# Kernel optimization log

Measured on AMD Instinct MI355X. Metric: run time of the kernel, lower is better.

## Reference

```python
import jax, jax.numpy as jnp
import numpy as np

B, C, F_IN, F_OUT = 4096, 63, 250, 250
NEG_SLOPE = 0.2  # GATConv default negative_slope


def setup_inputs() -> dict:
    key = jax.random.key(0)
    ks = jax.random.split(key, 5)
    return {
        "x": jax.random.normal(ks[0], (B, 1, C, F_IN), dtype=jnp.float32),
        "W": jax.random.normal(ks[1], (F_IN, F_OUT), dtype=jnp.float32) / np.sqrt(F_IN),
        "att_src": jax.random.normal(ks[2], (F_OUT,), dtype=jnp.float32) / np.sqrt(F_OUT),
        "att_dst": jax.random.normal(ks[3], (F_OUT,), dtype=jnp.float32) / np.sqrt(F_OUT),
        "bias": jax.random.normal(ks[4], (F_OUT,), dtype=jnp.float32) * 0.01,
    }


def reference(x, W, att_src, att_dst, bias):
    # x: [B, 1, C, F_in] -> per-batch graph of C=63 nodes, fully connected
    # (all i!=j edges plus GATConv's default self-loops => dense C x C attention).
    h = jnp.einsum("bcf,fo->bco", x[:, 0], W)          # [B, C, F_out] node embeddings
    a_s = jnp.einsum("bco,o->bc", h, att_src)           # per-source score
    a_d = jnp.einsum("bco,o->bc", h, att_dst)           # per-destination score
    # e[b, dst, src] = leakyrelu(a_s[src] + a_d[dst]); softmax over sources per dst
    e = jax.nn.leaky_relu(a_s[:, None, :] + a_d[:, :, None], NEG_SLOPE)  # [B, C, C]
    alpha = jax.nn.softmax(e, axis=-1)
    out = jnp.einsum("bds,bso->bdo", alpha, h) + bias   # [B, C, F_out]
    return out[:, None]                                  # [B, 1, C, F_out]
```

## Files before the change

kernel.cpp:

```cpp
#include <hip/hip_runtime.h>
#include <hip/hip_bf16.h>

typedef __bf16 bf16;
typedef __attribute__((ext_vector_type(8))) __bf16 bf16x8;
typedef __attribute__((ext_vector_type(2))) __bf16 bf16x2;
typedef __attribute__((ext_vector_type(4))) float f32x4;
typedef __attribute__((ext_vector_type(4))) unsigned int uint4v;

#define C_NODES 63
#define F_DIM   250
#define NEG_SLOPE 0.2f
#define BS 8

#define ROWB      1040
#define SLAB      0
#define OFF_AS    65536
#define OFF_AD    65792
#define ALPHA_B   66048
#define LDS_BYTES 74240

__device__ __forceinline__ int swz(int a) { return a ^ ((a >> 3) & 0x70); }

typedef const __attribute__((address_space(1))) void* gas_t;
typedef __attribute__((address_space(3))) void* las_t;
__device__ __forceinline__ void dma16(const void* g, void* l) {
    __builtin_amdgcn_global_load_lds((gas_t)g, (las_t)l, 16, 0, 0);
}

__device__ __forceinline__ void bar_lgkm() {
    asm volatile("s_waitcnt lgkmcnt(0)" ::: "memory");
    __builtin_amdgcn_s_barrier();
    __builtin_amdgcn_sched_barrier(0);
}

extern "C" __global__ __launch_bounds__(256)
void gat_prep(const float* __restrict__ W, const float* __restrict__ att_src,
              const float* __restrict__ att_dst, bf16* __restrict__ Wp) {
    int i = blockIdx.x * 256 + threadIdx.x;
    int tile = i >> 9;
    int ln   = (i >> 3) & 63;
    int j    = i & 7;
    int kt = tile >> 4, nt = tile & 15;
    int k = kt * 32 + (ln >> 4) * 8 + j;
    int n = nt * 16 + (ln & 15);
    float v = 0.f;
    if (k < F_DIM) {
        if (n < F_DIM) {
            v = W[k * F_DIM + n];
        } else if (n == F_DIM || n == F_DIM + 1) {
            const float* att = (n == F_DIM) ? att_src : att_dst;
            float s = 0.f;
            for (int o = 0; o < F_DIM; ++o) s = fmaf(W[k * F_DIM + o], att[o], s);
            v = s;
        }
    }
    Wp[i] = (bf16)v;
}

extern "C" __global__ __launch_bounds__(512, 4)
void gat_main(const float* __restrict__ x, const bf16* __restrict__ Wp,
              const float* __restrict__ bias, float* __restrict__ out)
{
    __shared__ __align__(16) unsigned char smem[LDS_BYTES];
    const int tid  = threadIdx.x;
    const int lane = tid & 63;
    const int w    = tid >> 6;
    const int fl   = lane & 15;
    const int fh   = lane >> 4;
    const int b0   = blockIdx.x * BS;

    const bf16x8* wpv = (const bf16x8*)Wp;

    float bv0, bv1;
    { int f = w * 32 + fl;      bv0 = (f < F_DIM) ? bias[f] : 0.f;
      f += 16;                  bv1 = (f < F_DIM) ? bias[f] : 0.f; }

    if (tid < 63) {
        *(unsigned long long*)(smem + SLAB + tid * ROWB + 1000) = 0ull;
        *(f32x4*)(smem + SLAB + tid * ROWB + 1008) = (f32x4){0.f, 0.f, 0.f, 0.f};
    }

    {
        const float* xb = x + (size_t)b0 * (C_NODES * F_DIM);
        float2 tl0 = {0.f, 0.f};
        if (tid < 63) tl0 = *(const float2*)(xb + tid * F_DIM + 248);
#pragma unroll
        for (int rr = 0; rr < 8; ++rr) {
            int r = w * 8 + rr;
            if (r < 63 && lane < 62)
                dma16(xb + r * F_DIM + lane * 4, smem + SLAB + r * ROWB);
        }
        if (tid < 63) *(float2*)(smem + SLAB + tid * ROWB + 992) = tl0;
    }
    asm volatile("s_waitcnt vmcnt(0)" ::: "memory");
    bar_lgkm();

#pragma unroll 1
    for (int i = 0; i < BS; ++i) {
        const int b = b0 + i;
        const float* xnext = x + (size_t)(b + 1) * (C_NODES * F_DIM);

        float2 tl = {0.f, 0.f};
        if (i + 1 < BS && tid < 63) tl = *(const float2*)(xnext + tid * F_DIM + 248);

        f32x4 gacc[4][2];
#pragma unroll
        for (int mt = 0; mt < 4; ++mt) {
            gacc[mt][0] = (f32x4){0.f, 0.f, 0.f, 0.f};
            gacc[mt][1] = (f32x4){0.f, 0.f, 0.f, 0.f};
        }
#pragma unroll 2
        for (int kt = 0; kt < 8; ++kt) {
            bf16x8 bw0 = wpv[(kt * 16 + w * 2)     * 64 + lane];
            bf16x8 bw1 = wpv[(kt * 16 + w * 2 + 1) * 64 + lane];
#pragma unroll
            for (int mt = 0; mt < 4; ++mt) {
                int row = mt * 16 + fl;
                bf16x8 af;
                if (row < C_NODES) {
                    const f32x4* p = (const f32x4*)(smem + SLAB + row * ROWB + kt * 128 + fh * 32);
                    f32x4 lo = p[0], hi = p[1];
                    af = (bf16x8){ (bf16)lo.x, (bf16)lo.y, (bf16)lo.z, (bf16)lo.w,
                                   (bf16)hi.x, (bf16)hi.y, (bf16)hi.z, (bf16)hi.w };
                } else {
                    af = (bf16x8){(bf16)0.f,(bf16)0.f,(bf16)0.f,(bf16)0.f,
                                  (bf16)0.f,(bf16)0.f,(bf16)0.f,(bf16)0.f};
                }
                gacc[mt][0] = __builtin_amdgcn_mfma_f32_16x16x32_bf16(af, bw0, gacc[mt][0], 0, 0, 0);
                gacc[mt][1] = __builtin_amdgcn_mfma_f32_16x16x32_bf16(af, bw1, gacc[mt][1], 0, 0, 0);
            }
        }
        if (w == 7 && (fl == 10 || fl == 11)) {
            float* dst = (float*)(smem + (fl == 10 ? OFF_AS : OFF_AD));
#pragma unroll
            for (int mt = 0; mt < 4; ++mt) {
                f32x4 v = gacc[mt][1];
#pragma unroll
                for (int q = 0; q < 4; ++q) dst[mt * 16 + fh * 4 + q] = v[q];
            }
        }
        bar_lgkm();

        if (i + 1 < BS) {
#pragma unroll
            for (int rr = 0; rr < 8; ++rr) {
                int r = w * 8 + rr;
                if (r < 63 && lane < 62)
                    dma16(xnext + r * F_DIM + lane * 4, smem + SLAB + r * ROWB);
            }
        }
        unsigned int pk[4][2][2];
#pragma unroll
        for (int mt = 0; mt < 4; ++mt)
#pragma unroll
            for (int nti = 0; nti < 2; ++nti) {
                f32x4 v = gacc[mt][nti];
                bf16x2 p0 = { (bf16)v.x, (bf16)v.y };
                bf16x2 p1 = { (bf16)v.z, (bf16)v.w };
                pk[mt][nti][0] = __builtin_bit_cast(unsigned int, p0);
                pk[mt][nti][1] = __builtin_bit_cast(unsigned int, p1);
            }
        const int LA = ((fh & 1) << 5) + fl;
        const int LB = LA + 16;
        const bool fhHi = (fh & 2) != 0;
        uint4v hb[2][2];
#pragma unroll
        for (int nti = 0; nti < 2; ++nti)
#pragma unroll
            for (int kt2 = 0; kt2 < 2; ++kt2) {
                unsigned int u[4];
#pragma unroll
                for (int h = 0; h < 2; ++h) {
                    unsigned int a0 = __shfl(pk[kt2 * 2][nti][h],     LA);
                    unsigned int a1 = __shfl(pk[kt2 * 2 + 1][nti][h], LA);
                    u[h] = fhHi ? a1 : a0;
                    unsigned int c0 = __shfl(pk[kt2 * 2][nti][h],     LB);
                    unsigned int c1 = __shfl(pk[kt2 * 2 + 1][nti][h], LB);
                    u[2 + h] = fhHi ? c1 : c0;
                }
                hb[nti][kt2] = (uint4v){u[0], u[1], u[2], u[3]};
            }
        {
            const float* AS  = (const float*)(smem + OFF_AS);
            const float* ADp = (const float*)(smem + OFF_AD);
            int d = tid >> 3;
            int c = tid & 7;
            float ad_v = ADp[d];
            f32x4 a0 = *(const f32x4*)(AS + c * 8);
            f32x4 a1 = *(const f32x4*)(AS + c * 8 + 4);
            float p[8];
#pragma unroll
            for (int k = 0; k < 4; ++k) {
                float e;
                e = a0[k] + ad_v; p[k]     = (e > 0.f) ? e : NEG_SLOPE * e;
                e = a1[k] + ad_v; p[4 + k] = (e > 0.f) ? e : NEG_SLOPE * e;
            }
            if (c == 7) p[7] = -3.0e38f;
            float md = p[0];
#pragma unroll
            for (int k = 1; k < 8; ++k) md = fmaxf(md, p[k]);
            md = fmaxf(md, __shfl_xor(md, 1));
            md = fmaxf(md, __shfl_xor(md, 2));
            md = fmaxf(md, __shfl_xor(md, 4));
            float sum = 0.f;
#pragma unroll
            for (int k = 0; k < 8; ++k) { p[k] = __expf(p[k] - md); sum += p[k]; }
            sum += __shfl_xor(sum, 1);
            sum += __shfl_xor(sum, 2);
            sum += __shfl_xor(sum, 4);
            float rz = 1.f / sum;
            bf16x8 pkv;
#pragma unroll
            for (int k = 0; k < 8; ++k) pkv[k] = (bf16)(p[k] * rz);
            *(bf16x8*)(smem + swz(ALPHA_B + d * 128 + c * 16)) = pkv;
        }
        if (i + 1 < BS && tid < 63)
            *(float2*)(smem + SLAB + tid * ROWB + 992) = tl;
        bar_lgkm();

#pragma unroll
        for (int mt = 0; mt < 4; ++mt) {
            gacc[mt][0] = (f32x4){0.f, 0.f, 0.f, 0.f};
            gacc[mt][1] = (f32x4){0.f, 0.f, 0.f, 0.f};
        }
#pragma unroll
        for (int ks = 0; ks < 2; ++ks) {
            int kk = ks * 32 + fh * 8;
            bf16x8 h0 = __builtin_bit_cast(bf16x8, hb[0][ks]);
            bf16x8 h1 = __builtin_bit_cast(bf16x8, hb[1][ks]);
#pragma unroll
            for (int mt = 0; mt < 4; ++mt) {
                bf16x8 aal = *(const bf16x8*)(smem + swz(ALPHA_B + (mt * 16 + fl) * 128 + kk * 2));
                gacc[mt][0] = __builtin_amdgcn_mfma_f32_16x16x32_bf16(aal, h0, gacc[mt][0], 0, 0, 0);
                gacc[mt][1] = __builtin_amdgcn_mfma_f32_16x16x32_bf16(aal, h1, gacc[mt][1], 0, 0, 0);
            }
        }
        float* ob = out + (size_t)b * (C_NODES * F_DIM);
#pragma unroll
        for (int mt = 0; mt < 4; ++mt) {
#pragma unroll
            for (int q = 0; q < 4; ++q) {
                int r = mt * 16 + fh * 4 + q;
                if (r < C_NODES) {
                    int f = w * 32 + fl;
                    ob[r * F_DIM + f] = gacc[mt][0][q] + bv0;
                    f += 16;
                    if (f < F_DIM) ob[r * F_DIM + f] = gacc[mt][1][q] + bv1;
                }
            }
        }
        if (i + 1 < BS) {
            asm volatile("s_waitcnt vmcnt(32)" ::: "memory");
            bar_lgkm();
        }
    }
}

extern "C" void kernel_launch(void* const* d_in, const int* in_sizes, int n_in,
                              void* d_out, int out_size, void* d_ws, size_t ws_size,
                              hipStream_t stream) {
    const float* x       = (const float*)d_in[0];
    const float* W       = (const float*)d_in[1];
    const float* att_src = (const float*)d_in[2];
    const float* att_dst = (const float*)d_in[3];
    const float* bias    = (const float*)d_in[4];
    float* out = (float*)d_out;
    bf16* Wp = (bf16*)d_ws;

    gat_prep<<<256, 256, 0, stream>>>(W, att_src, att_dst, Wp);
    gat_main<<<512, 512, 0, stream>>>(x, Wp, bias, out);
}
```

Baseline: 139.6 us.

## Double-buffer x slabs and software-pipeline the next graph's projection GEMM

Adds a second LDS slab so x for graph i+2 is DMA'd while graph i is processed. The projection GEMM for the next graph is moved to the end of the current iteration, after the attention GEMM. Graphs per block rise from 8 to 16 and the grid is halved, aiming to hide global-load latency behind compute. LDS per block roughly doubles and launch bounds drop to 2, so fewer blocks fit per CU. The explicit vmcnt waits before the slabs are read are removed, which risks reading LDS before the DMA has landed.

```diff
diff --git a/kernel.cpp b/kernel.cpp
--- a/kernel.cpp
+++ b/kernel.cpp
@@ -10,14 +10,15 @@
 #define C_NODES 63
 #define F_DIM   250
 #define NEG_SLOPE 0.2f
-#define BS 8
+#define BS 16
 
 #define ROWB      1040
-#define SLAB      0
-#define OFF_AS    65536
-#define OFF_AD    65792
-#define ALPHA_B   66048
-#define LDS_BYTES 74240
+#define SLAB0     0
+#define SLAB1     65536
+#define OFF_AS    131072
+#define OFF_AD    131328
+#define ALPHA_B   131584
+#define LDS_BYTES 139776
 
 __device__ __forceinline__ int swz(int a) { return a ^ ((a >> 3) & 0x70); }
 
@@ -57,7 +58,7 @@
     Wp[i] = (bf16)v;
 }
 
-extern "C" __global__ __launch_bounds__(512, 4)
+extern "C" __global__ __launch_bounds__(512, 2)
 void gat_main(const float* __restrict__ x, const bf16* __restrict__ Wp,
               const float* __restrict__ bias, float* __restrict__ out)
 {
@@ -76,8 +77,10 @@
       f += 16;                  bv1 = (f < F_DIM) ? bias[f] : 0.f; }
 
     if (tid < 63) {
-        *(unsigned long long*)(smem + SLAB + tid * ROWB + 1000) = 0ull;
-        *(f32x4*)(smem + SLAB + tid * ROWB + 1008) = (f32x4){0.f, 0.f, 0.f, 0.f};
+        *(unsigned long long*)(smem + SLAB0 + tid * ROWB + 1000) = 0ull;
+        *(f32x4*)(smem + SLAB0 + tid * ROWB + 1008) = (f32x4){0.f, 0.f, 0.f, 0.f};
+        *(unsigned long long*)(smem + SLAB1 + tid * ROWB + 1000) = 0ull;
+        *(f32x4*)(smem + SLAB1 + tid * ROWB + 1008) = (f32x4){0.f, 0.f, 0.f, 0.f};
     }
 
     {
@@ -88,65 +91,78 @@
         for (int rr = 0; rr < 8; ++rr) {
             int r = w * 8 + rr;
             if (r < 63 && lane < 62)
-                dma16(xb + r * F_DIM + lane * 4, smem + SLAB + r * ROWB);
-        }
-        if (tid < 63) *(float2*)(smem + SLAB + tid * ROWB + 992) = tl0;
-    }
-    asm volatile("s_waitcnt vmcnt(0)" ::: "memory");
+                dma16(xb + r * F_DIM + lane * 4, smem + SLAB0 + r * ROWB);
+        }
+        if (tid < 63) *(float2*)(smem + SLAB0 + tid * ROWB + 992) = tl0;
+    }
+    {
+        const float* xb = x + (size_t)(b0 + 1) * (C_NODES * F_DIM);
+        float2 tl1 = {0.f, 0.f};
+        if (tid < 63) tl1 = *(const float2*)(xb + tid * F_DIM + 248);
+#pragma unroll
+        for (int rr = 0; rr < 8; ++rr) {
+            int r = w * 8 + rr;
+            if (r < 63 && lane < 62)
+                dma16(xb + r * F_DIM + lane * 4, smem + SLAB1 + r * ROWB);
+        }
+        if (tid < 63) *(float2*)(smem + SLAB1 + tid * ROWB + 992) = tl1;
+    }
+    bar_lgkm();
+
+    f32x4 gacc[4][2];
+#pragma unroll
+    for (int mt = 0; mt < 4; ++mt) {
+        gacc[mt][0] = (f32x4){0.f, 0.f, 0.f, 0.f};
+        gacc[mt][1] = (f32x4){0.f, 0.f, 0.f, 0.f};
+    }
+#pragma unroll 2
+    for (int kt = 0; kt < 8; ++kt) {
+        bf16x8 bw0 = wpv[(kt * 16 + w * 2)     * 64 + lane];
+        bf16x8 bw1 = wpv[(kt * 16 + w * 2 + 1) * 64 + lane];
+#pragma unroll
+        for (int mt = 0; mt < 4; ++mt) {
+            int row = mt * 16 + fl;
+            bf16x8 af;
+            if (row < C_NODES) {
+                const f32x4* p = (const f32x4*)(smem + SLAB0 + row * ROWB + kt * 128 + fh * 32);
+                f32x4 lo = p[0], hi = p[1];
+                af = (bf16x8){ (bf16)lo.x, (bf16)lo.y, (bf16)lo.z, (bf16)lo.w,
+                               (bf16)hi.x, (bf16)hi.y, (bf16)hi.z, (bf16)hi.w };
+            } else {
+                af = (bf16x8){(bf16)0.f,(bf16)0.f,(bf16)0.f,(bf16)0.f,
+                              (bf16)0.f,(bf16)0.f,(bf16)0.f,(bf16)0.f};
+            }
+            gacc[mt][0] = __builtin_amdgcn_mfma_f32_16x16x32_bf16(af, bw0, gacc[mt][0], 0, 0, 0);
+            gacc[mt][1] = __builtin_amdgcn_mfma_f32_16x16x32_bf16(af, bw1, gacc[mt][1], 0, 0, 0);
+        }
+    }
+    if (w == 7 && (fl == 10 || fl == 11)) {
+        float* dst = (float*)(smem + (fl == 10 ? OFF_AS : OFF_AD));
+#pragma unroll
+        for (int mt = 0; mt < 4; ++mt) {
+            f32x4 v = gacc[mt][1];
+#pragma unroll
+            for (int q = 0; q < 4; ++q) dst[mt * 16 + fh * 4 + q] = v[q];
+        }
+    }
     bar_lgkm();
 
 #pragma unroll 1
     for (int i = 0; i < BS; ++i) {
         const int b = b0 + i;
-        const float* xnext = x + (size_t)(b + 1) * (C_NODES * F_DIM);
+        const int slabNext = ((i + 1) & 1) ? SLAB1 : SLAB0;
+        const int slabDma  = (i & 1) ? SLAB1 : SLAB0;
 
         float2 tl = {0.f, 0.f};
-        if (i + 1 < BS && tid < 63) tl = *(const float2*)(xnext + tid * F_DIM + 248);
-
-        f32x4 gacc[4][2];
-#pragma unroll
-        for (int mt = 0; mt < 4; ++mt) {
-            gacc[mt][0] = (f32x4){0.f, 0.f, 0.f, 0.f};
-            gacc[mt][1] = (f32x4){0.f, 0.f, 0.f, 0.f};
-        }
-#pragma unroll 2
-        for (int kt = 0; kt < 8; ++kt) {
-            bf16x8 bw0 = wpv[(kt * 16 + w * 2)     * 64 + lane];
-            bf16x8 bw1 = wpv[(kt * 16 + w * 2 + 1) * 64 + lane];
-#pragma unroll
-            for (int mt = 0; mt < 4; ++mt) {
-                int row = mt * 16 + fl;
-                bf16x8 af;
-                if (row < C_NODES) {
-                    const f32x4* p = (const f32x4*)(smem + SLAB + row * ROWB + kt * 128 + fh * 32);
-                    f32x4 lo = p[0], hi = p[1];
-                    af = (bf16x8){ (bf16)lo.x, (bf16)lo.y, (bf16)lo.z, (bf16)lo.w,
-                                   (bf16)hi.x, (bf16)hi.y, (bf16)hi.z, (bf16)hi.w };
-                } else {
-                    af = (bf16x8){(bf16)0.f,(bf16)0.f,(bf16)0.f,(bf16)0.f,
-                                  (bf16)0.f,(bf16)0.f,(bf16)0.f,(bf16)0.f};
-                }
-                gacc[mt][0] = __builtin_amdgcn_mfma_f32_16x16x32_bf16(af, bw0, gacc[mt][0], 0, 0, 0);
-                gacc[mt][1] = __builtin_amdgcn_mfma_f32_16x16x32_bf16(af, bw1, gacc[mt][1], 0, 0, 0);
-            }
-        }
-        if (w == 7 && (fl == 10 || fl == 11)) {
-            float* dst = (float*)(smem + (fl == 10 ? OFF_AS : OFF_AD));
-#pragma unroll
-            for (int mt = 0; mt < 4; ++mt) {
-                f32x4 v = gacc[mt][1];
-#pragma unroll
-                for (int q = 0; q < 4; ++q) dst[mt * 16 + fh * 4 + q] = v[q];
-            }
-        }
-        bar_lgkm();
-
-        if (i + 1 < BS) {
+        const bool dmaEn = (i + 2 < BS);
+        if (dmaEn) {
+            const float* xn = x + (size_t)(b + 2) * (C_NODES * F_DIM);
+            if (tid < 63) tl = *(const float2*)(xn + tid * F_DIM + 248);
 #pragma unroll
             for (int rr = 0; rr < 8; ++rr) {
                 int r = w * 8 + rr;
                 if (r < 63 && lane < 62)
-                    dma16(xnext + r * F_DIM + lane * 4, smem + SLAB + r * ROWB);
+                    dma16(xn + r * F_DIM + lane * 4, smem + slabDma + r * ROWB);
             }
         }
         unsigned int pk[4][2][2];
@@ -214,8 +230,11 @@
             for (int k = 0; k < 8; ++k) pkv[k] = (bf16)(p[k] * rz);
             *(bf16x8*)(smem + swz(ALPHA_B + d * 128 + c * 16)) = pkv;
         }
-        if (i + 1 < BS && tid < 63)
-            *(float2*)(smem + SLAB + tid * ROWB + 992) = tl;
+        if (dmaEn) {
+            if (tid < 63) *(float2*)(smem + slabDma + tid * ROWB + 992) = tl;
+        } else if (i + 1 < BS) {
+            asm volatile("s_waitcnt vmcnt(0)" ::: "memory");
+        }
         bar_lgkm();
 
 #pragma unroll
@@ -250,9 +269,43 @@
             }
         }
         if (i + 1 < BS) {
-            asm volatile("s_waitcnt vmcnt(32)" ::: "memory");
-            bar_lgkm();
-        }
+#pragma unroll
+            for (int mt = 0; mt < 4; ++mt) {
+                gacc[mt][0] = (f32x4){0.f, 0.f, 0.f, 0.f};
+                gacc[mt][1] = (f32x4){0.f, 0.f, 0.f, 0.f};
+            }
+#pragma unroll 2
+            for (int kt = 0; kt < 8; ++kt) {
+                bf16x8 bw0 = wpv[(kt * 16 + w * 2)     * 64 + lane];
+                bf16x8 bw1 = wpv[(kt * 16 + w * 2 + 1) * 64 + lane];
+#pragma unroll
+                for (int mt = 0; mt < 4; ++mt) {
+                    int row = mt * 16 + fl;
+                    bf16x8 af;
+                    if (row < C_NODES) {
+                        const f32x4* p = (const f32x4*)(smem + slabNext + row * ROWB + kt * 128 + fh * 32);
+                        f32x4 lo = p[0], hi = p[1];
+                        af = (bf16x8){ (bf16)lo.x, (bf16)lo.y, (bf16)lo.z, (bf16)lo.w,
+                                       (bf16)hi.x, (bf16)hi.y, (bf16)hi.z, (bf16)hi.w };
+                    } else {
+                        af = (bf16x8){(bf16)0.f,(bf16)0.f,(bf16)0.f,(bf16)0.f,
+                                      (bf16)0.f,(bf16)0.f,(bf16)0.f,(bf16)0.f};
+                    }
+                    gacc[mt][0] = __builtin_amdgcn_mfma_f32_16x16x32_bf16(af, bw0, gacc[mt][0], 0, 0, 0);
+                    gacc[mt][1] = __builtin_amdgcn_mfma_f32_16x16x32_bf16(af, bw1, gacc[mt][1], 0, 0, 0);
+                }
+            }
+            if (w == 7 && (fl == 10 || fl == 11)) {
+                float* dst = (float*)(smem + (fl == 10 ? OFF_AS : OFF_AD));
+#pragma unroll
+                for (int mt = 0; mt < 4; ++mt) {
+                    f32x4 v = gacc[mt][1];
+#pragma unroll
+                    for (int q = 0; q < 4; ++q) dst[mt * 16 + fh * 4 + q] = v[q];
+                }
+            }
+        }
+        bar_lgkm();
     }
 }
 
@@ -268,5 +321,5 @@
     bf16* Wp = (bf16*)d_ws;
 
     gat_prep<<<256, 256, 0, stream>>>(W, att_src, att_dst, Wp);
-    gat_main<<<512, 512, 0, stream>>>(x, Wp, bias, out);
-}
+    gat_main<<<256, 512, 0, stream>>>(x, Wp, bias, out);
+}
```

Result: slower. 144.4 us (+3.4%).

## Stage x as bf16 MFMA fragments in LDS and transpose h through LDS

Applied to the files above, without the earlier changes.

After each DMA of x, every wave converts its own fp32 rows once into a swizzled bf16 fragment layout in LDS, so the first GEMM loads A operands directly instead of converting fp32 on every k-step. The cross-lane shuffle transpose of h is replaced by a bf16 store to and reload from a swizzled LDS buffer. The batch count per block is doubled while the grid is halved. LDS use nearly doubles, which cuts resident blocks per CU and reduces latency hiding, and the per-row conversion adds an extra pass over LDS.

```diff
diff --git a/kernel.cpp b/kernel.cpp
--- a/kernel.cpp
+++ b/kernel.cpp
@@ -3,23 +3,28 @@
 
 typedef __bf16 bf16;
 typedef __attribute__((ext_vector_type(8))) __bf16 bf16x8;
+typedef __attribute__((ext_vector_type(4))) __bf16 bf16x4;
 typedef __attribute__((ext_vector_type(2))) __bf16 bf16x2;
 typedef __attribute__((ext_vector_type(4))) float f32x4;
-typedef __attribute__((ext_vector_type(4))) unsigned int uint4v;
 
 #define C_NODES 63
 #define F_DIM   250
 #define NEG_SLOPE 0.2f
-#define BS 8
+#define BS 16
 
 #define ROWB      1040
 #define SLAB      0
-#define OFF_AS    65536
-#define OFF_AD    65792
-#define ALPHA_B   66048
-#define LDS_BYTES 74240
+#define AFR_B     65536
+#define HSB       98304
+#define OFF_AS    130304
+#define OFF_AD    130560
+#define ALPHA_B   131072
+#define LDS_BYTES 139264
 
 __device__ __forceinline__ int swz(int a) { return a ^ ((a >> 3) & 0x70); }
+__device__ __forceinline__ int swzA(int a) {
+    return a ^ ((((a >> 8) & 3) ^ ((a >> 10) & 3)) << 4) ^ (((a >> 12) & 1) << 6);
+}
 
 typedef const __attribute__((address_space(1))) void* gas_t;
 typedef __attribute__((address_space(3))) void* las_t;
@@ -31,6 +36,22 @@
     asm volatile("s_waitcnt lgkmcnt(0)" ::: "memory");
     __builtin_amdgcn_s_barrier();
     __builtin_amdgcn_sched_barrier(0);
+}
+
+__device__ __forceinline__ void conv_rows(unsigned char* smem, int w, int lane) {
+#pragma unroll
+    for (int rr = 0; rr < 8; ++rr) {
+        int r = w * 8 + rr;
+        if (r < C_NODES) {
+            f32x4 v = *(const f32x4*)(smem + SLAB + r * ROWB + lane * 16);
+            int c = lane * 4;
+            int dl = (r & 15) | (((c >> 3) & 3) << 4);
+            int base = AFR_B + swzA((((r >> 4) * 8 + (c >> 5)) << 10)
+                                    + dl * 16 + (c & 4) * 2);
+            bf16x4 o = { (bf16)v.x, (bf16)v.y, (bf16)v.z, (bf16)v.w };
+            *(bf16x4*)(smem + base) = o;
+        }
+    }
 }
 
 extern "C" __global__ __launch_bounds__(256)
@@ -57,7 +78,7 @@
     Wp[i] = (bf16)v;
 }
 
-extern "C" __global__ __launch_bounds__(512, 4)
+extern "C" __global__ __launch_bounds__(512, 2)
 void gat_main(const float* __restrict__ x, const bf16* __restrict__ Wp,
               const float* __restrict__ bias, float* __restrict__ out)
 {
@@ -78,6 +99,10 @@
     if (tid < 63) {
         *(unsigned long long*)(smem + SLAB + tid * ROWB + 1000) = 0ull;
         *(f32x4*)(smem + SLAB + tid * ROWB + 1008) = (f32x4){0.f, 0.f, 0.f, 0.f};
+    } else if (tid < 96) {
+        int idx = tid - 64;
+        int base = AFR_B + swzA(((24 + (idx >> 2)) << 10) + ((((idx & 3) << 4) | 15) * 16));
+        *(f32x4*)(smem + base) = (f32x4){0.f, 0.f, 0.f, 0.f};
     }
 
     {
@@ -93,15 +118,15 @@
         if (tid < 63) *(float2*)(smem + SLAB + tid * ROWB + 992) = tl0;
     }
     asm volatile("s_waitcnt vmcnt(0)" ::: "memory");
+    __syncthreads();
+    conv_rows(smem, w, lane);
     bar_lgkm();
 
 #pragma unroll 1
     for (int i = 0; i < BS; ++i) {
         const int b = b0 + i;
+        const bool pfen = (i + 1 < BS);
         const float* xnext = x + (size_t)(b + 1) * (C_NODES * F_DIM);
-
-        float2 tl = {0.f, 0.f};
-        if (i + 1 < BS && tid < 63) tl = *(const float2*)(xnext + tid * F_DIM + 248);
 
         f32x4 gacc[4][2];
 #pragma unroll
@@ -115,17 +140,8 @@
             bf16x8 bw1 = wpv[(kt * 16 + w * 2 + 1) * 64 + lane];
 #pragma unroll
             for (int mt = 0; mt < 4; ++mt) {
-                int row = mt * 16 + fl;
-                bf16x8 af;
-                if (row < C_NODES) {
-                    const f32x4* p = (const f32x4*)(smem + SLAB + row * ROWB + kt * 128 + fh * 32);
-                    f32x4 lo = p[0], hi = p[1];
-                    af = (bf16x8){ (bf16)lo.x, (bf16)lo.y, (bf16)lo.z, (bf16)lo.w,
-                                   (bf16)hi.x, (bf16)hi.y, (bf16)hi.z, (bf16)hi.w };
-                } else {
-                    af = (bf16x8){(bf16)0.f,(bf16)0.f,(bf16)0.f,(bf16)0.f,
-                                  (bf16)0.f,(bf16)0.f,(bf16)0.f,(bf16)0.f};
-                }
+                bf16x8 af = *(const bf16x8*)(smem + AFR_B
+                                + swzA(((mt * 8 + kt) << 10) + lane * 16));
                 gacc[mt][0] = __builtin_amdgcn_mfma_f32_16x16x32_bf16(af, bw0, gacc[mt][0], 0, 0, 0);
                 gacc[mt][1] = __builtin_amdgcn_mfma_f32_16x16x32_bf16(af, bw1, gacc[mt][1], 0, 0, 0);
             }
@@ -141,7 +157,9 @@
         }
         bar_lgkm();
 
-        if (i + 1 < BS) {
+        float2 tl = {0.f, 0.f};
+        if (pfen) {
+            if (tid < 63) tl = *(const float2*)(xnext + tid * F_DIM + 248);
 #pragma unroll
             for (int rr = 0; rr < 8; ++rr) {
                 int r = w * 8 + rr;
@@ -149,37 +167,19 @@
                     dma16(xnext + r * F_DIM + lane * 4, smem + SLAB + r * ROWB);
             }
         }
-        unsigned int pk[4][2][2];
-#pragma unroll
-        for (int mt = 0; mt < 4; ++mt)
+#pragma unroll
+        for (int mt = 0; mt < 4; ++mt) {
+            int s0 = mt * 16 + fh * 4;
 #pragma unroll
             for (int nti = 0; nti < 2; ++nti) {
-                f32x4 v = gacc[mt][nti];
-                bf16x2 p0 = { (bf16)v.x, (bf16)v.y };
-                bf16x2 p1 = { (bf16)v.z, (bf16)v.w };
-                pk[mt][nti][0] = __builtin_bit_cast(unsigned int, p0);
-                pk[mt][nti][1] = __builtin_bit_cast(unsigned int, p1);
-            }
-        const int LA = ((fh & 1) << 5) + fl;
-        const int LB = LA + 16;
-        const bool fhHi = (fh & 2) != 0;
-        uint4v hb[2][2];
-#pragma unroll
-        for (int nti = 0; nti < 2; ++nti)
-#pragma unroll
-            for (int kt2 = 0; kt2 < 2; ++kt2) {
-                unsigned int u[4];
-#pragma unroll
-                for (int h = 0; h < 2; ++h) {
-                    unsigned int a0 = __shfl(pk[kt2 * 2][nti][h],     LA);
-                    unsigned int a1 = __shfl(pk[kt2 * 2 + 1][nti][h], LA);
-                    u[h] = fhHi ? a1 : a0;
-                    unsigned int c0 = __shfl(pk[kt2 * 2][nti][h],     LB);
-                    unsigned int c1 = __shfl(pk[kt2 * 2 + 1][nti][h], LB);
-                    u[2 + h] = fhHi ? c1 : c0;
+                int f = w * 32 + nti * 16 + fl;
+                if (f < F_DIM) {
+                    f32x4 v = gacc[mt][nti];
+                    bf16x4 hv = { (bf16)v.x, (bf16)v.y, (bf16)v.z, (bf16)v.w };
+                    *(bf16x4*)(smem + swz(HSB + f * 128 + s0 * 2)) = hv;
                 }
-                hb[nti][kt2] = (uint4v){u[0], u[1], u[2], u[3]};
-            }
+            }
+        }
         {
             const float* AS  = (const float*)(smem + OFF_AS);
             const float* ADp = (const float*)(smem + OFF_AD);
@@ -214,7 +214,7 @@
             for (int k = 0; k < 8; ++k) pkv[k] = (bf16)(p[k] * rz);
             *(bf16x8*)(smem + swz(ALPHA_B + d * 128 + c * 16)) = pkv;
         }
-        if (i + 1 < BS && tid < 63)
+        if (pfen && tid < 63)
             *(float2*)(smem + SLAB + tid * ROWB + 992) = tl;
         bar_lgkm();
 
@@ -226,13 +226,13 @@
 #pragma unroll
         for (int ks = 0; ks < 2; ++ks) {
             int kk = ks * 32 + fh * 8;
-            bf16x8 h0 = __builtin_bit_cast(bf16x8, hb[0][ks]);
-            bf16x8 h1 = __builtin_bit_cast(bf16x8, hb[1][ks]);
+            bf16x8 hbf0 = *(const bf16x8*)(smem + swz(HSB + (w * 32 + fl)      * 128 + kk * 2));
+            bf16x8 hbf1 = *(const bf16x8*)(smem + swz(HSB + (w * 32 + fl + 16) * 128 + kk * 2));
 #pragma unroll
             for (int mt = 0; mt < 4; ++mt) {
                 bf16x8 aal = *(const bf16x8*)(smem + swz(ALPHA_B + (mt * 16 + fl) * 128 + kk * 2));
-                gacc[mt][0] = __builtin_amdgcn_mfma_f32_16x16x32_bf16(aal, h0, gacc[mt][0], 0, 0, 0);
-                gacc[mt][1] = __builtin_amdgcn_mfma_f32_16x16x32_bf16(aal, h1, gacc[mt][1], 0, 0, 0);
+                gacc[mt][0] = __builtin_amdgcn_mfma_f32_16x16x32_bf16(aal, hbf0, gacc[mt][0], 0, 0, 0);
+                gacc[mt][1] = __builtin_amdgcn_mfma_f32_16x16x32_bf16(aal, hbf1, gacc[mt][1], 0, 0, 0);
             }
         }
         float* ob = out + (size_t)b * (C_NODES * F_DIM);
@@ -249,10 +249,11 @@
                 }
             }
         }
-        if (i + 1 < BS) {
+        if (pfen) {
             asm volatile("s_waitcnt vmcnt(32)" ::: "memory");
-            bar_lgkm();
-        }
+            conv_rows(smem, w, lane);
+        }
+        bar_lgkm();
     }
 }
 
@@ -268,5 +269,5 @@
     bf16* Wp = (bf16*)d_ws;
 
     gat_prep<<<256, 256, 0, stream>>>(W, att_src, att_dst, Wp);
-    gat_main<<<512, 512, 0, stream>>>(x, Wp, bias, out);
-}
+    gat_main<<<256, 512, 0, stream>>>(x, Wp, bias, out);
+}
```

After: 133.8 us (median of 2 runs). -4.2%, faster.

## Process two graphs per iteration to reuse W fragments and halve barriers

Applied to the files above, without the earlier changes.

Each block now loads two batch graphs at a time into a doubled LDS slab and runs 8-row-tile MFMA GEMMs, so every W fragment read from global is used for twice as many rows and barriers per graph are halved. The softmax is remapped to four threads per destination row per graph, and the grid shrinks to 256 blocks of 16 graphs each. LDS per block roughly doubles and launch bounds drop to 2 blocks per CU, which cuts occupancy and raises register pressure from the doubled accumulators.

```diff
diff --git a/kernel.cpp b/kernel.cpp
--- a/kernel.cpp
+++ b/kernel.cpp
@@ -9,15 +9,16 @@
 
 #define C_NODES 63
 #define F_DIM   250
+#define CF      (C_NODES * F_DIM)
 #define NEG_SLOPE 0.2f
-#define BS 8
+#define NP 8
 
 #define ROWB      1040
 #define SLAB      0
-#define OFF_AS    65536
-#define OFF_AD    65792
-#define ALPHA_B   66048
-#define LDS_BYTES 74240
+#define ALPHA_B   131072
+#define OFF_AS    147456
+#define OFF_AD    147712
+#define LDS_BYTES 148480
 
 __device__ __forceinline__ int swz(int a) { return a ^ ((a >> 3) & 0x70); }
 
@@ -57,7 +58,7 @@
     Wp[i] = (bf16)v;
 }
 
-extern "C" __global__ __launch_bounds__(512, 4)
+extern "C" __global__ __launch_bounds__(512, 2)
 void gat_main(const float* __restrict__ x, const bf16* __restrict__ Wp,
               const float* __restrict__ bias, float* __restrict__ out)
 {
@@ -67,7 +68,7 @@
     const int w    = tid >> 6;
     const int fl   = lane & 15;
     const int fh   = lane >> 4;
-    const int b0   = blockIdx.x * BS;
+    const int b0   = blockIdx.x * (2 * NP);
 
     const bf16x8* wpv = (const bf16x8*)Wp;
 
@@ -75,37 +76,42 @@
     { int f = w * 32 + fl;      bv0 = (f < F_DIM) ? bias[f] : 0.f;
       f += 16;                  bv1 = (f < F_DIM) ? bias[f] : 0.f; }
 
-    if (tid < 63) {
+    if (tid < 126) {
         *(unsigned long long*)(smem + SLAB + tid * ROWB + 1000) = 0ull;
         *(f32x4*)(smem + SLAB + tid * ROWB + 1008) = (f32x4){0.f, 0.f, 0.f, 0.f};
     }
 
     {
-        const float* xb = x + (size_t)b0 * (C_NODES * F_DIM);
+        const float* xa = x + (size_t)b0 * CF;
+        const float* xb2 = x + (size_t)(b0 + 1) * CF;
         float2 tl0 = {0.f, 0.f};
-        if (tid < 63) tl0 = *(const float2*)(xb + tid * F_DIM + 248);
-#pragma unroll
-        for (int rr = 0; rr < 8; ++rr) {
-            int r = w * 8 + rr;
-            if (r < 63 && lane < 62)
-                dma16(xb + r * F_DIM + lane * 4, smem + SLAB + r * ROWB);
-        }
-        if (tid < 63) *(float2*)(smem + SLAB + tid * ROWB + 992) = tl0;
+        if (tid < 126) {
+            const float* s = (tid < 63) ? (xa + tid * F_DIM)
+                                        : (xb2 + (tid - 63) * F_DIM);
+            tl0 = *(const float2*)(s + 248);
+        }
+#pragma unroll
+        for (int rr = 0; rr < 16; ++rr) {
+            int r = w * 16 + rr;
+            if (r < 126 && lane < 62) {
+                const float* s = (r < 63) ? (xa + r * F_DIM)
+                                          : (xb2 + (r - 63) * F_DIM);
+                dma16(s + lane * 4, smem + SLAB + r * ROWB);
+            }
+        }
+        if (tid < 126) *(float2*)(smem + SLAB + tid * ROWB + 992) = tl0;
     }
     asm volatile("s_waitcnt vmcnt(0)" ::: "memory");
-    bar_lgkm();
+    __syncthreads();
 
 #pragma unroll 1
-    for (int i = 0; i < BS; ++i) {
-        const int b = b0 + i;
-        const float* xnext = x + (size_t)(b + 1) * (C_NODES * F_DIM);
-
-        float2 tl = {0.f, 0.f};
-        if (i + 1 < BS && tid < 63) tl = *(const float2*)(xnext + tid * F_DIM + 248);
-
-        f32x4 gacc[4][2];
-#pragma unroll
-        for (int mt = 0; mt < 4; ++mt) {
+    for (int j = 0; j < NP; ++j) {
+        const int b = b0 + 2 * j;
+        const bool pfen = (j + 1 < NP);
+
+        f32x4 gacc[8][2];
+#pragma unroll
+        for (int mt = 0; mt < 8; ++mt) {
             gacc[mt][0] = (f32x4){0.f, 0.f, 0.f, 0.f};
             gacc[mt][1] = (f32x4){0.f, 0.f, 0.f, 0.f};
         }
@@ -114,11 +120,12 @@
             bf16x8 bw0 = wpv[(kt * 16 + w * 2)     * 64 + lane];
             bf16x8 bw1 = wpv[(kt * 16 + w * 2 + 1) * 64 + lane];
 #pragma unroll
-            for (int mt = 0; mt < 4; ++mt) {
-                int row = mt * 16 + fl;
+            for (int mt = 0; mt < 8; ++mt) {
+                int lr = (mt & 3) * 16 + fl;
+                int sr = lr + (mt >> 2) * 63;
                 bf16x8 af;
-                if (row < C_NODES) {
-                    const f32x4* p = (const f32x4*)(smem + SLAB + row * ROWB + kt * 128 + fh * 32);
+                if (lr < C_NODES) {
+                    const f32x4* p = (const f32x4*)(smem + SLAB + sr * ROWB + kt * 128 + fh * 32);
                     f32x4 lo = p[0], hi = p[1];
                     af = (bf16x8){ (bf16)lo.x, (bf16)lo.y, (bf16)lo.z, (bf16)lo.w,
                                    (bf16)hi.x, (bf16)hi.y, (bf16)hi.z, (bf16)hi.w };
@@ -131,128 +138,157 @@
             }
         }
         if (w == 7 && (fl == 10 || fl == 11)) {
-            float* dst = (float*)(smem + (fl == 10 ? OFF_AS : OFF_AD));
-#pragma unroll
-            for (int mt = 0; mt < 4; ++mt) {
+#pragma unroll
+            for (int mt = 0; mt < 8; ++mt) {
+                float* dst = (float*)(smem + (fl == 10 ? OFF_AS : OFF_AD) + (mt >> 2) * 512);
                 f32x4 v = gacc[mt][1];
 #pragma unroll
-                for (int q = 0; q < 4; ++q) dst[mt * 16 + fh * 4 + q] = v[q];
+                for (int q = 0; q < 4; ++q)
+                    dst[(mt & 3) * 16 + fh * 4 + q] = v[q];
             }
         }
         bar_lgkm();
 
-        if (i + 1 < BS) {
-#pragma unroll
-            for (int rr = 0; rr < 8; ++rr) {
-                int r = w * 8 + rr;
-                if (r < 63 && lane < 62)
-                    dma16(xnext + r * F_DIM + lane * 4, smem + SLAB + r * ROWB);
-            }
-        }
-        unsigned int pk[4][2][2];
-#pragma unroll
-        for (int mt = 0; mt < 4; ++mt)
-#pragma unroll
-            for (int nti = 0; nti < 2; ++nti) {
-                f32x4 v = gacc[mt][nti];
-                bf16x2 p0 = { (bf16)v.x, (bf16)v.y };
-                bf16x2 p1 = { (bf16)v.z, (bf16)v.w };
-                pk[mt][nti][0] = __builtin_bit_cast(unsigned int, p0);
-                pk[mt][nti][1] = __builtin_bit_cast(unsigned int, p1);
-            }
+        float2 tl = {0.f, 0.f};
+        if (pfen) {
+            const float* xa = x + (size_t)(b + 2) * CF;
+            const float* xb2 = x + (size_t)(b + 3) * CF;
+            if (tid < 126) {
+                const float* s = (tid < 63) ? (xa + tid * F_DIM)
+                                            : (xb2 + (tid - 63) * F_DIM);
+                tl = *(const float2*)(s + 248);
+            }
+#pragma unroll
+            for (int rr = 0; rr < 16; ++rr) {
+                int r = w * 16 + rr;
+                if (r < 126 && lane < 62) {
+                    const float* s = (r < 63) ? (xa + r * F_DIM)
+                                              : (xb2 + (r - 63) * F_DIM);
+                    dma16(s + lane * 4, smem + SLAB + r * ROWB);
+                }
+            }
+        }
         const int LA = ((fh & 1) << 5) + fl;
         const int LB = LA + 16;
         const bool fhHi = (fh & 2) != 0;
-        uint4v hb[2][2];
-#pragma unroll
-        for (int nti = 0; nti < 2; ++nti)
-#pragma unroll
-            for (int kt2 = 0; kt2 < 2; ++kt2) {
-                unsigned int u[4];
-#pragma unroll
-                for (int h = 0; h < 2; ++h) {
-                    unsigned int a0 = __shfl(pk[kt2 * 2][nti][h],     LA);
-                    unsigned int a1 = __shfl(pk[kt2 * 2 + 1][nti][h], LA);
-                    u[h] = fhHi ? a1 : a0;
-                    unsigned int c0 = __shfl(pk[kt2 * 2][nti][h],     LB);
-                    unsigned int c1 = __shfl(pk[kt2 * 2 + 1][nti][h], LB);
-                    u[2 + h] = fhHi ? c1 : c0;
-                }
-                hb[nti][kt2] = (uint4v){u[0], u[1], u[2], u[3]};
-            }
+        uint4v hb[2][2][2];
+#pragma unroll
+        for (int h = 0; h < 2; ++h) {
+            unsigned int pk[4][2][2];
+#pragma unroll
+            for (int mt4 = 0; mt4 < 4; ++mt4)
+#pragma unroll
+                for (int nti = 0; nti < 2; ++nti) {
+                    f32x4 v = gacc[h * 4 + mt4][nti];
+                    bf16x2 p0 = { (bf16)v.x, (bf16)v.y };
+                    bf16x2 p1 = { (bf16)v.z, (bf16)v.w };
+                    pk[mt4][nti][0] = __builtin_bit_cast(unsigned int, p0);
+                    pk[mt4][nti][1] = __builtin_bit_cast(unsigned int, p1);
+                }
+#pragma unroll
+            for (int nti = 0; nti < 2; ++nti)
+#pragma unroll
+                for (int kt2 = 0; kt2 < 2; ++kt2) {
+                    unsigned int u[4];
+#pragma unroll
+                    for (int hh = 0; hh < 2; ++hh) {
+                        unsigned int a0 = __shfl(pk[kt2 * 2][nti][hh],     LA);
+                        unsigned int a1 = __shfl(pk[kt2 * 2 + 1][nti][hh], LA);
+                        u[hh] = fhHi ? a1 : a0;
+                        unsigned int c0 = __shfl(pk[kt2 * 2][nti][hh],     LB);
+                        unsigned int c1 = __shfl(pk[kt2 * 2 + 1][nti][hh], LB);
+                        u[2 + hh] = fhHi ? c1 : c0;
+                    }
+                    hb[h][nti][kt2] = (uint4v){u[0], u[1], u[2], u[3]};
+                }
+        }
         {
-            const float* AS  = (const float*)(smem + OFF_AS);
-            const float* ADp = (const float*)(smem + OFF_AD);
-            int d = tid >> 3;
-            int c = tid & 7;
+            int half = tid >> 8;
+            int d    = (tid >> 2) & 63;
+            int c    = tid & 3;
+            const float* AS  = (const float*)(smem + OFF_AS + half * 512);
+            const float* ADp = (const float*)(smem + OFF_AD + half * 512);
             float ad_v = ADp[d];
-            f32x4 a0 = *(const f32x4*)(AS + c * 8);
-            f32x4 a1 = *(const f32x4*)(AS + c * 8 + 4);
-            float p[8];
+            f32x4 s0 = *(const f32x4*)(AS + c * 16);
+            f32x4 s1 = *(const f32x4*)(AS + c * 16 + 4);
+            f32x4 s2 = *(const f32x4*)(AS + c * 16 + 8);
+            f32x4 s3 = *(const f32x4*)(AS + c * 16 + 12);
+            float p[16];
 #pragma unroll
             for (int k = 0; k < 4; ++k) {
                 float e;
-                e = a0[k] + ad_v; p[k]     = (e > 0.f) ? e : NEG_SLOPE * e;
-                e = a1[k] + ad_v; p[4 + k] = (e > 0.f) ? e : NEG_SLOPE * e;
-            }
-            if (c == 7) p[7] = -3.0e38f;
+                e = s0[k] + ad_v; p[k]      = (e > 0.f) ? e : NEG_SLOPE * e;
+                e = s1[k] + ad_v; p[4 + k]  = (e > 0.f) ? e : NEG_SLOPE * e;
+                e = s2[k] + ad_v; p[8 + k]  = (e > 0.f) ? e : NEG_SLOPE * e;
+                e = s3[k] + ad_v; p[12 + k] = (e > 0.f) ? e : NEG_SLOPE * e;
+            }
+            if (c == 3) p[15] = -3.0e38f;
             float md = p[0];
 #pragma unroll
-            for (int k = 1; k < 8; ++k) md = fmaxf(md, p[k]);
+            for (int k = 1; k < 16; ++k) md = fmaxf(md, p[k]);
             md = fmaxf(md, __shfl_xor(md, 1));
             md = fmaxf(md, __shfl_xor(md, 2));
-            md = fmaxf(md, __shfl_xor(md, 4));
             float sum = 0.f;
 #pragma unroll
-            for (int k = 0; k < 8; ++k) { p[k] = __expf(p[k] - md); sum += p[k]; }
+            for (int k = 0; k < 16; ++k) { p[k] = __expf(p[k] - md); sum += p[k]; }
             sum += __shfl_xor(sum, 1);
             sum += __shfl_xor(sum, 2);
-            sum += __shfl_xor(sum, 4);
             float rz = 1.f / sum;
-            bf16x8 pkv;
-#pragma unroll
-            for (int k = 0; k < 8; ++k) pkv[k] = (bf16)(p[k] * rz);
-            *(bf16x8*)(smem + swz(ALPHA_B + d * 128 + c * 16)) = pkv;
-        }
-        if (i + 1 < BS && tid < 63)
+            bf16x8 pk0, pk1;
+#pragma unroll
+            for (int k = 0; k < 8; ++k) {
+                pk0[k] = (bf16)(p[k] * rz);
+                pk1[k] = (bf16)(p[8 + k] * rz);
+            }
+            int base = ALPHA_B + half * 8192 + d * 128 + c * 32;
+            *(bf16x8*)(smem + swz(base))      = pk0;
+            *(bf16x8*)(smem + swz(base + 16)) = pk1;
+        }
+        if (pfen && tid < 126)
             *(float2*)(smem + SLAB + tid * ROWB + 992) = tl;
         bar_lgkm();
 
 #pragma unroll
-        for (int mt = 0; mt < 4; ++mt) {
+        for (int mt = 0; mt < 8; ++mt) {
             gacc[mt][0] = (f32x4){0.f, 0.f, 0.f, 0.f};
             gacc[mt][1] = (f32x4){0.f, 0.f, 0.f, 0.f};
         }
 #pragma unroll
-        for (int ks = 0; ks < 2; ++ks) {
-            int kk = ks * 32 + fh * 8;
-            bf16x8 h0 = __builtin_bit_cast(bf16x8, hb[0][ks]);
-            bf16x8 h1 = __builtin_bit_cast(bf16x8, hb[1][ks]);
-#pragma unroll
-            for (int mt = 0; mt < 4; ++mt) {
-                bf16x8 aal = *(const bf16x8*)(smem + swz(ALPHA_B + (mt * 16 + fl) * 128 + kk * 2));
-                gacc[mt][0] = __builtin_amdgcn_mfma_f32_16x16x32_bf16(aal, h0, gacc[mt][0], 0, 0, 0);
-                gacc[mt][1] = __builtin_amdgcn_mfma_f32_16x16x32_bf16(aal, h1, gacc[mt][1], 0, 0, 0);
-            }
-        }
-        float* ob = out + (size_t)b * (C_NODES * F_DIM);
-#pragma unroll
-        for (int mt = 0; mt < 4; ++mt) {
-#pragma unroll
-            for (int q = 0; q < 4; ++q) {
-                int r = mt * 16 + fh * 4 + q;
-                if (r < C_NODES) {
-                    int f = w * 32 + fl;
-                    ob[r * F_DIM + f] = gacc[mt][0][q] + bv0;
-                    f += 16;
-                    if (f < F_DIM) ob[r * F_DIM + f] = gacc[mt][1][q] + bv1;
-                }
-            }
-        }
-        if (i + 1 < BS) {
-            asm volatile("s_waitcnt vmcnt(32)" ::: "memory");
-            bar_lgkm();
-        }
+        for (int h = 0; h < 2; ++h)
+#pragma unroll
+            for (int ks = 0; ks < 2; ++ks) {
+                int kk = ks * 32 + fh * 8;
+                bf16x8 h0 = __builtin_bit_cast(bf16x8, hb[h][0][ks]);
+                bf16x8 h1 = __builtin_bit_cast(bf16x8, hb[h][1][ks]);
+#pragma unroll
+                for (int mt4 = 0; mt4 < 4; ++mt4) {
+                    bf16x8 aal = *(const bf16x8*)(smem + swz(ALPHA_B + h * 8192
+                                        + (mt4 * 16 + fl) * 128 + kk * 2));
+                    gacc[h * 4 + mt4][0] = __builtin_amdgcn_mfma_f32_16x16x32_bf16(aal, h0, gacc[h * 4 + mt4][0], 0, 0, 0);
+                    gacc[h * 4 + mt4][1] = __builtin_amdgcn_mfma_f32_16x16x32_bf16(aal, h1, gacc[h * 4 + mt4][1], 0, 0, 0);
+                }
+            }
+#pragma unroll
+        for (int h = 0; h < 2; ++h) {
+            float* ob = out + (size_t)(b + h) * CF;
+#pragma unroll
+            for (int mt4 = 0; mt4 < 4; ++mt4) {
+#pragma unroll
+                for (int q = 0; q < 4; ++q) {
+                    int r = mt4 * 16 + fh * 4 + q;
+                    if (r < C_NODES) {
+                        int f = w * 32 + fl;
+                        ob[r * F_DIM + f] = gacc[h * 4 + mt4][0][q] + bv0;
+                        f += 16;
+                        if (f < F_DIM) ob[r * F_DIM + f] = gacc[h * 4 + mt4][1][q] + bv1;
+                    }
+                }
+            }
+        }
+        if (pfen) {
+            asm volatile("s_waitcnt vmcnt(63)" ::: "memory");
+        }
+        bar_lgkm();
     }
 }
 
@@ -268,5 +304,5 @@
     bf16* Wp = (bf16*)d_ws;
 
     gat_prep<<<256, 256, 0, stream>>>(W, att_src, att_dst, Wp);
-    gat_main<<<512, 512, 0, stream>>>(x, Wp, bias, out);
-}
+    gat_main<<<256, 512, 0, stream>>>(x, Wp, bias, out);
+}
```

New measurement: 158.1 us. +13.2%, slower.
